# Performance work log

Hardware: AMD Instinct MI355X
Metric: run time of the kernel (lower is better)

Reference implementation:

```python
import jax, jax.numpy as jnp
import numpy as np
from jax import lax

D_MODEL = 768
D_STATE = 16
D_CONV = 4
EXPAND = 2
D_INNER = EXPAND * D_MODEL  # 1536
DT_RANK = (D_MODEL + 15) // 16  # 48
BATCH = 4
SEQ_LEN = 2048


def setup_inputs() -> dict:
    key = jax.random.key(0)
    ks = jax.random.split(key, 8)
    x = jax.random.normal(ks[0], (BATCH, SEQ_LEN, D_MODEL), dtype=jnp.float32)
    W_in = jax.random.normal(ks[1], (D_INNER * 2, D_MODEL), dtype=jnp.float32) * 0.02
    conv_w = jax.random.normal(ks[2], (D_INNER, 1, D_CONV), dtype=jnp.float32) * 0.1
    conv_b = jnp.zeros((D_INNER,), dtype=jnp.float32)
    W_x = jax.random.normal(ks[3], (DT_RANK + 2 * D_STATE, D_INNER), dtype=jnp.float32) * 0.02
    dt_std = DT_RANK ** -0.5
    W_dt = jax.random.uniform(ks[4], (D_INNER, DT_RANK), minval=-dt_std, maxval=dt_std, dtype=jnp.float32)
    b_dt = jnp.zeros((D_INNER,), dtype=jnp.float32)
    A_log = jnp.log(jnp.tile(jnp.arange(1, D_STATE + 1, dtype=jnp.float32), (D_INNER, 1)))
    D_param = jnp.ones((D_INNER,), dtype=jnp.float32)
    W_out = jax.random.normal(ks[5], (D_MODEL, D_INNER), dtype=jnp.float32) * 0.02
    return {"x": x, "W_in": W_in, "conv_w": conv_w, "conv_b": conv_b,
            "W_x": W_x, "W_dt": W_dt, "b_dt": b_dt, "A_log": A_log,
            "D_param": D_param, "W_out": W_out}


def _silu(v):
    return v * jax.nn.sigmoid(v)


def reference(x, W_in, conv_w, conv_b, W_x, W_dt, b_dt, A_log, D_param, W_out):
    B, L, _ = x.shape
    # in_proj and split into x-branch / gate z
    xz = jnp.einsum('bld,ed->ble', x, W_in)            # (B, L, 2*d_inner)
    xb, z = jnp.split(xz, 2, axis=-1)
    # depthwise causal conv1d (torch pads both sides then truncates to L)
    xc = jnp.transpose(xb, (0, 2, 1))                   # (B, d_inner, L)
    xc = lax.conv_general_dilated(xc, conv_w, window_strides=(1,),
                                  padding=[(D_CONV - 1, 0)],
                                  feature_group_count=D_INNER,
                                  dimension_numbers=('NCH', 'OIH', 'NCH'))
    xc = xc + conv_b[None, :, None]
    xc = jnp.transpose(xc, (0, 2, 1))                   # (B, L, d_inner)
    xc = _silu(xc)
    # ssm input-dependent params
    x_dbl = jnp.einsum('bld,ed->ble', xc, W_x)          # (B, L, dt_rank+2*d_state)
    dt_r = x_dbl[..., :DT_RANK]
    Bm = x_dbl[..., DT_RANK:DT_RANK + D_STATE]          # (B, L, d_state)
    Cm = x_dbl[..., DT_RANK + D_STATE:]
    dt = jax.nn.softplus(jnp.einsum('blr,dr->bld', dt_r, W_dt) + b_dt)
    A = -jnp.exp(A_log)                                 # (d_inner, d_state)
    # selective scan over time
    def step(h, inp):
        x_t, dt_t, B_t, C_t = inp                       # (B,d_inner),(B,d_inner),(B,d_state),(B,d_state)
        dA = jnp.exp(dt_t[..., None] * A)               # (B, d_inner, d_state)
        h = dA * h + (dt_t * x_t)[..., None] * B_t[:, None, :]
        y_t = jnp.einsum('bdn,bn->bd', h, C_t) + D_param * x_t
        return h, y_t
    h0 = jnp.zeros((B, D_INNER, D_STATE), dtype=x.dtype)
    xs = (jnp.transpose(xc, (1, 0, 2)), jnp.transpose(dt, (1, 0, 2)),
          jnp.transpose(Bm, (1, 0, 2)), jnp.transpose(Cm, (1, 0, 2)))
    _, ys = lax.scan(step, h0, xs)                      # (L, B, d_inner)
    y = jnp.transpose(ys, (1, 0, 2))
    y = y * _silu(z)
    return jnp.einsum('bld,od->blo', y, W_out)
```

## Files before the change

### kernel.cpp

```cpp
#include <hip/hip_runtime.h>
#include <hip/hip_bf16.h>
#include <math.h>

#define D_MODEL   768
#define D_STATE   16
#define D_CONV    4
#define D_INNER   1536
#define DT_RANK   48
#define BATCH     4
#define SEQ_LEN   2048
#define BL        (BATCH * SEQ_LEN)
#define NCHUNK    32
#define CHUNK     (SEQ_LEN / NCHUNK)

typedef __bf16 bf16x8 __attribute__((ext_vector_type(8)));
typedef float  f32x4  __attribute__((ext_vector_type(4)));

__device__ __forceinline__ void async_copy16(const void* g, void* l) {
    __builtin_amdgcn_global_load_lds(
        (const __attribute__((address_space(1))) void*)g,
        (__attribute__((address_space(3))) void*)l,
        16, 0, 0);
}


#define SYNC_V6 do { asm volatile("s_waitcnt vmcnt(6)" ::: "memory"); \
    __builtin_amdgcn_s_barrier(); __builtin_amdgcn_sched_barrier(0); } while (0)
#define SYNC_V4 do { asm volatile("s_waitcnt vmcnt(4)" ::: "memory"); \
    __builtin_amdgcn_s_barrier(); __builtin_amdgcn_sched_barrier(0); } while (0)
#define SYNC_V2 do { asm volatile("s_waitcnt vmcnt(2)" ::: "memory"); \
    __builtin_amdgcn_s_barrier(); __builtin_amdgcn_sched_barrier(0); } while (0)
#define SYNC_V0 do { asm volatile("s_waitcnt vmcnt(0)" ::: "memory"); \
    __builtin_amdgcn_s_barrier(); __builtin_amdgcn_sched_barrier(0); } while (0)
#define SYNC_B  do { \
    __builtin_amdgcn_s_barrier(); __builtin_amdgcn_sched_barrier(0); } while (0)

template<int IH, int JH>
__device__ __forceinline__ void quad24(f32x4 (&acc)[2][4][2][2],
                                       const bf16x8 (&aH)[4], const bf16x8 (&aL)[4],
                                       const bf16x8 (&bH)[2], const bf16x8 (&bL)[2])
{
    __builtin_amdgcn_s_setprio(1);
    #pragma unroll
    for (int i = 0; i < 4; ++i)
        #pragma unroll
        for (int j = 0; j < 2; ++j) {
            acc[IH][i][JH][j] = __builtin_amdgcn_mfma_f32_16x16x32_bf16(aH[i], bH[j], acc[IH][i][JH][j], 0, 0, 0);
            acc[IH][i][JH][j] = __builtin_amdgcn_mfma_f32_16x16x32_bf16(aH[i], bL[j], acc[IH][i][JH][j], 0, 0, 0);
            acc[IH][i][JH][j] = __builtin_amdgcn_mfma_f32_16x16x32_bf16(aL[i], bH[j], acc[IH][i][JH][j], 0, 0, 0);
        }
    __builtin_amdgcn_s_setprio(0);
}

__global__ __launch_bounds__(512, 2)
void gemm256(const __bf16* __restrict__ A, const __bf16* __restrict__ B,
             float* __restrict__ C, int K, int ldc)
{
    __shared__ __bf16 Asl0[256 * 64];
    __shared__ __bf16 Bsl0[256 * 64];
    __shared__ __bf16 Asl1[256 * 64];
    __shared__ __bf16 Bsl1[256 * 64];

    const int tid  = threadIdx.x;
    const int lane = tid & 63;
    const int w    = tid >> 6;
    const int aw   = (w >> 2) * 64;
    const int bw   = (w & 3) * 32;

    const int bm = blockIdx.y * 256;
    const int bn = blockIdx.x * 256;

    const long lda = 2L * K;
    const long ldb = 2L * K;

    f32x4 acc[2][4][2][2];
    #pragma unroll
    for (int a = 0; a < 2; ++a)
        #pragma unroll
        for (int i = 0; i < 4; ++i)
            #pragma unroll
            for (int b = 0; b < 2; ++b)
                #pragma unroll
                for (int j = 0; j < 2; ++j)
                    acc[a][i][b][j] = (f32x4){0.f, 0.f, 0.f, 0.f};

    const int srow = w * 8 + (lane >> 3);
    const int q    = (lane & 7) ^ ((lane >> 3) & 7);
    const int qoff = (q < 4) ? q * 8 : K + (q - 4) * 8;
    const __bf16* Ab = A + (long)(bm + srow) * lda + qoff;
    const __bf16* Bb = B + (long)(bn + srow) * ldb + qoff;
    const long lda64 = 64 * lda, ldb64 = 64 * ldb;
    const int wo = w * 1024;

    const int fr = lane & 15;
    const int g4 = lane >> 4;

    const int nt = K >> 5;

    __bf16 *Ac = Asl0, *Bc = Bsl0, *An = Asl1, *Bn = Bsl1;

    auto stA = [&](int kk, __bf16* dst, int half) {
        char* d = (char*)dst + half * 16384 + wo;
        const __bf16* s = Ab + kk + (long)(2 * half) * lda64;
        async_copy16(s, d);
        async_copy16(s + lda64, d + 8192);
    };
    auto stB = [&](int kk, __bf16* dst, int half) {
        char* d = (char*)dst + half * 16384 + wo;
        const __bf16* s = Bb + kk + (long)(2 * half) * ldb64;
        async_copy16(s, d);
        async_copy16(s + ldb64, d + 8192);
    };
    auto rdA = [&](const __bf16* As, int ih, bf16x8 (&aH)[4], bf16x8 (&aL)[4]) {
        #pragma unroll
        for (int t = 0; t < 4; ++t) {
            const int ra = aw + ih * 128 + t * 16 + fr;
            aH[t] = *(const bf16x8*)&As[ra * 64 + ((g4       ^ (ra & 7)) * 8)];
            aL[t] = *(const bf16x8*)&As[ra * 64 + (((4 + g4) ^ (ra & 7)) * 8)];
        }
    };
    auto rdB = [&](const __bf16* Bs, int jh, bf16x8 (&bH)[2], bf16x8 (&bL)[2]) {
        #pragma unroll
        for (int t = 0; t < 2; ++t) {
            const int rb = bw + jh * 128 + t * 16 + fr;
            bH[t] = *(const bf16x8*)&Bs[rb * 64 + ((g4       ^ (rb & 7)) * 8)];
            bL[t] = *(const bf16x8*)&Bs[rb * 64 + (((4 + g4) ^ (rb & 7)) * 8)];
        }
    };

    stA(0, Ac, 0);
    stB(0, Bc, 0);
    stB(0, Bc, 1);
    stA(0, Ac, 1);
    SYNC_V4;

    for (int t = 0; t < nt - 1; ++t) {
        const int kk1 = (t + 1) * 32;
        bf16x8 aH[4], aL[4], bH[2], bL[2];
        rdA(Ac, 0, aH, aL);
        rdB(Bc, 0, bH, bL);
        stA(kk1, An, 0);
        SYNC_V6;
        quad24<0, 0>(acc, aH, aL, bH, bL);
        rdB(Bc, 1, bH, bL);
        stB(kk1, Bn, 0);
        SYNC_V6;
        quad24<0, 1>(acc, aH, aL, bH, bL);
        rdA(Ac, 1, aH, aL);
        stB(kk1, Bn, 1);
        SYNC_V6;
        quad24<1, 1>(acc, aH, aL, bH, bL);
        rdB(Bc, 0, bH, bL);
        stA(kk1, An, 1);
        SYNC_B;
        quad24<1, 0>(acc, aH, aL, bH, bL);
        __bf16* tp;
        tp = Ac; Ac = An; An = tp;
        tp = Bc; Bc = Bn; Bn = tp;
    }

    {
        bf16x8 aH[4], aL[4], bH[2], bL[2];
        rdA(Ac, 0, aH, aL);
        rdB(Bc, 0, bH, bL);
        SYNC_V4;
        quad24<0, 0>(acc, aH, aL, bH, bL);
        rdB(Bc, 1, bH, bL);
        SYNC_V2;
        quad24<0, 1>(acc, aH, aL, bH, bL);
        rdA(Ac, 1, aH, aL);
        SYNC_V0;
        quad24<1, 1>(acc, aH, aL, bH, bL);
        rdB(Bc, 0, bH, bL);
        quad24<1, 0>(acc, aH, aL, bH, bL);
    }

    const int cn  = lane & 15;
    const int cr4 = (lane >> 4) * 4;
    #pragma unroll
    for (int ih = 0; ih < 2; ++ih)
        #pragma unroll
        for (int i = 0; i < 4; ++i)
            #pragma unroll
            for (int jh = 0; jh < 2; ++jh)
                #pragma unroll
                for (int j = 0; j < 2; ++j)
                    #pragma unroll
                    for (int r = 0; r < 4; ++r) {
                        const int row = bm + aw + ih * 128 + i * 16 + cr4 + r;
                        const int col = bn + bw + jh * 128 + j * 16 + cn;
                        C[(long)row * ldc + col] = acc[ih][i][jh][j][r];
                    }
}

template <int EPI>
__global__ __launch_bounds__(256)
void gemm_f(const __bf16* __restrict__ A, const __bf16* __restrict__ B,
            float* __restrict__ C, const float* __restrict__ bias,
            int M, int N, int K, int ldc)
{
    __shared__ __bf16 Asl[128 * 64];
    __shared__ __bf16 Bsl[128 * 64];

    const int tid  = threadIdx.x;
    const int lane = tid & 63;
    const int w    = tid >> 6;
    const int wm   = (w >> 1) * 64;
    const int wn   = (w & 1) * 64;

    const int bm = blockIdx.y * 128;
    const int bn = blockIdx.x * 128;

    const long lda = 2L * K;
    const long ldb = 2L * K;

    f32x4 acc[4][4];
    #pragma unroll
    for (int i = 0; i < 4; ++i)
        #pragma unroll
        for (int j = 0; j < 4; ++j)
            acc[i][j] = (f32x4){0.f, 0.f, 0.f, 0.f};

    const int srow = w * 32 + (lane >> 3);
    const int q    = (lane & 7) ^ ((lane >> 3) & 7);
    const int qoff = (q < 4) ? q * 8 : K + (q - 4) * 8;
    const __bf16* Abase = A + (long)(bm + srow) * lda + qoff;
    const __bf16* Bbase = B + (long)(bn + srow) * ldb + qoff;
    char* AslW = (char*)Asl + (w * 32) * 128;
    char* BslW = (char*)Bsl + (w * 32) * 128;

    const int fr = lane & 15;
    const int g4 = lane >> 4;
    const long lda8 = 8 * lda, ldb8 = 8 * ldb;

    for (int kk = 0; kk < K; kk += 32) {
        __syncthreads();
        #pragma unroll
        for (int j = 0; j < 4; ++j) {
            async_copy16(Abase + j * lda8 + kk, AslW + j * 1024);
            async_copy16(Bbase + j * ldb8 + kk, BslW + j * 1024);
        }
        __syncthreads();

        bf16x8 ah[4], al[4], bh[4], bl[4];
        #pragma unroll
        for (int t = 0; t < 4; ++t) {
            const int ra = wm + t * 16 + fr;
            const int rb = wn + t * 16 + fr;
            ah[t] = *(const bf16x8*)&Asl[ra * 64 + ((g4       ^ (ra & 7)) * 8)];
            al[t] = *(const bf16x8*)&Asl[ra * 64 + (((4 + g4) ^ (ra & 7)) * 8)];
            bh[t] = *(const bf16x8*)&Bsl[rb * 64 + ((g4       ^ (rb & 7)) * 8)];
            bl[t] = *(const bf16x8*)&Bsl[rb * 64 + (((4 + g4) ^ (rb & 7)) * 8)];
        }
        #pragma unroll
        for (int i = 0; i < 4; ++i)
            #pragma unroll
            for (int j = 0; j < 4; ++j) {
                acc[i][j] = __builtin_amdgcn_mfma_f32_16x16x32_bf16(ah[i], bh[j], acc[i][j], 0, 0, 0);
                acc[i][j] = __builtin_amdgcn_mfma_f32_16x16x32_bf16(ah[i], bl[j], acc[i][j], 0, 0, 0);
                acc[i][j] = __builtin_amdgcn_mfma_f32_16x16x32_bf16(al[i], bh[j], acc[i][j], 0, 0, 0);
            }
    }

    const int cn  = lane & 15;
    const int cr4 = (lane >> 4) * 4;
    #pragma unroll
    for (int i = 0; i < 4; ++i)
        #pragma unroll
        for (int j = 0; j < 4; ++j)
            #pragma unroll
            for (int r = 0; r < 4; ++r) {
                const int row = bm + wm + i * 16 + cr4 + r;
                const int col = bn + wn + j * 16 + cn;
                float v = acc[i][j][r];
                if (EPI == 1) {
                    v += bias[col];
                    v = fmaxf(v, 0.f) + log1pf(__expf(-fabsf(v)));
                }
                C[(long)row * ldc + col] = v;
            }
}

__global__ __launch_bounds__(256)
void gemm_xdbl(const __bf16* __restrict__ A, const __bf16* __restrict__ B,
               float* __restrict__ xdtP, float* __restrict__ xbc)
{
    __shared__ __bf16 Asl[128 * 64];
    __shared__ __bf16 Bsl[128 * 64];

    const int tid  = threadIdx.x;
    const int lane = tid & 63;
    const int w    = tid >> 6;
    const int wm   = (w >> 1) * 64;
    const int wn   = (w & 1) * 64;

    const int s  = blockIdx.x;
    const int bm = blockIdx.y * 128;
    const int K  = 1536;
    const long lda = 3072, ldb = 3072;

    f32x4 acc[4][4];
    #pragma unroll
    for (int i = 0; i < 4; ++i)
        #pragma unroll
        for (int j = 0; j < 4; ++j)
            acc[i][j] = (f32x4){0.f, 0.f, 0.f, 0.f};

    const int srow = w * 32 + (lane >> 3);
    const int q    = (lane & 7) ^ ((lane >> 3) & 7);
    const int qoff = (q < 4) ? q * 8 : K + (q - 4) * 8;
    const __bf16* Abase = A + (long)(bm + srow) * lda + qoff;
    const __bf16* Bbase = B + (long)srow * ldb + qoff;
    char* AslW = (char*)Asl + (w * 32) * 128;
    char* BslW = (char*)Bsl + (w * 32) * 128;

    const int fr = lane & 15;
    const int g4 = lane >> 4;
    const long lda8 = 8 * lda, ldb8 = 8 * ldb;

    for (int kt = s * 12; kt < (s + 1) * 12; ++kt) {
        const int kk = kt * 32;
        __syncthreads();
        #pragma unroll
        for (int j = 0; j < 4; ++j) {
            async_copy16(Abase + j * lda8 + kk, AslW + j * 1024);
            async_copy16(Bbase + j * ldb8 + kk, BslW + j * 1024);
        }
        __syncthreads();

        bf16x8 ah[4], al[4], bh[4], bl[4];
        #pragma unroll
        for (int t = 0; t < 4; ++t) {
            const int ra = wm + t * 16 + fr;
            const int rb = wn + t * 16 + fr;
            ah[t] = *(const bf16x8*)&Asl[ra * 64 + ((g4       ^ (ra & 7)) * 8)];
            al[t] = *(const bf16x8*)&Asl[ra * 64 + (((4 + g4) ^ (ra & 7)) * 8)];
            bh[t] = *(const bf16x8*)&Bsl[rb * 64 + ((g4       ^ (rb & 7)) * 8)];
            bl[t] = *(const bf16x8*)&Bsl[rb * 64 + (((4 + g4) ^ (rb & 7)) * 8)];
        }
        #pragma unroll
        for (int i = 0; i < 4; ++i)
            #pragma unroll
            for (int j = 0; j < 4; ++j) {
                acc[i][j] = __builtin_amdgcn_mfma_f32_16x16x32_bf16(ah[i], bh[j], acc[i][j], 0, 0, 0);
                acc[i][j] = __builtin_amdgcn_mfma_f32_16x16x32_bf16(ah[i], bl[j], acc[i][j], 0, 0, 0);
                acc[i][j] = __builtin_amdgcn_mfma_f32_16x16x32_bf16(al[i], bh[j], acc[i][j], 0, 0, 0);
            }
    }

    const int cn  = lane & 15;
    const int cr4 = (lane >> 4) * 4;
    #pragma unroll
    for (int i = 0; i < 4; ++i)
        #pragma unroll
        for (int j = 0; j < 4; ++j) {
            const int col = wn + j * 16 + cn;
            if (col >= 80) continue;
            #pragma unroll
            for (int r = 0; r < 4; ++r) {
                const int row = bm + wm + i * 16 + cr4 + r;
                const float v = acc[i][j][r];
                if (col < 48) atomicAdd(&xdtP[(long)row * 48 + col], v);
                else          atomicAdd(&xbc [(long)row * 32 + (col - 48)], v);
            }
        }
}

__global__ __launch_bounds__(256)
void zero_xp(float* __restrict__ xbc, float* __restrict__ xdtP)
{
    const long i = (long)blockIdx.x * 256 + threadIdx.x;
    if (i < 8192L * 32) xbc[i]  = 0.f;
    if (i < 8192L * 48) xdtP[i] = 0.f;
}

__global__ __launch_bounds__(256)
void xdt_split(const float* __restrict__ xdtP, __bf16* __restrict__ xdtS)
{
    const long i = (long)blockIdx.x * 256 + threadIdx.x;
    if (i >= 8192L * 128) return;
    const long r = i >> 7;
    const int  c = (int)(i & 127);
    const int  k = c & 63;
    const float u = (k < 48) ? xdtP[r * 48 + k] : 0.f;
    const __bf16 hi = (__bf16)u;
    xdtS[i] = (c < 64) ? hi : (__bf16)(u - (float)hi);
}

#define NW0 ((long)BL * 768)
#define NW1 (3072L * 768)
#define NW2 (768L * 1536)
#define NW3 (80L * 1536)
#define NW4 (1536L * 128)
__global__ __launch_bounds__(256)
void split_all(const float* __restrict__ x,
               const float* __restrict__ W_in, const float* __restrict__ W_out,
               const float* __restrict__ W_x, const float* __restrict__ W_dt,
               __bf16* __restrict__ xS,
               __bf16* __restrict__ wInS, __bf16* __restrict__ wOutS,
               __bf16* __restrict__ wXS, __bf16* __restrict__ wDtS)
{
    long i = (long)blockIdx.x * 256 + threadIdx.x;
    if (i < NW0) {
        const long row = i / 768; const int col = (int)(i - row * 768);
        const float a = x[i];
        const __bf16 h = (__bf16)a;
        __bf16* d = xS + row * 1536 + col;
        d[0] = h; d[768] = (__bf16)(a - (float)h);
        return;
    }
    i -= NW0;
    if (i < NW1) {
        const long row = i / 768; const int col = (int)(i - row * 768);
        const float a = W_in[i];
        const __bf16 h = (__bf16)a;
        __bf16* d = wInS + row * 1536 + col;
        d[0] = h; d[768] = (__bf16)(a - (float)h);
        return;
    }
    i -= NW1;
    if (i < NW2) {
        const long row = i / 1536; const int col = (int)(i - row * 1536);
        const float a = W_out[i];
        const __bf16 h = (__bf16)a;
        __bf16* d = wOutS + row * 3072 + col;
        d[0] = h; d[1536] = (__bf16)(a - (float)h);
        return;
    }
    i -= NW2;
    if (i < NW3) {
        const long row = i / 1536; const int col = (int)(i - row * 1536);
        const float a = W_x[i];
        const __bf16 h = (__bf16)a;
        __bf16* d = wXS + row * 3072 + col;
        d[0] = h; d[1536] = (__bf16)(a - (float)h);
        return;
    }
    i -= NW3;
    if (i < NW4) {
        const long row = i >> 7; const int c = (int)(i & 127);
        const int k = c & 63;
        const float a = (k < 48) ? W_dt[row * 48 + k] : 0.f;
        const __bf16 h = (__bf16)a;
        wDtS[row * 128 + c] = (c < 64) ? h : (__bf16)(a - (float)h);
    }
}

typedef __bf16 bf16x4 __attribute__((ext_vector_type(4)));

__global__ __launch_bounds__(256)
void conv_silu_kernel(const float* __restrict__ xz,
                      const float* __restrict__ conv_w,
                      const float* __restrict__ conv_b,
                      __bf16* __restrict__ xcS)
{
    const long idx = (long)blockIdx.x * 256 + threadIdx.x;
    const int d4 = (int)(idx % (D_INNER / 4)) * 4;
    const long bl = idx / (D_INNER / 4);
    const int l  = (int)(bl % SEQ_LEN);

    const f32x4 w0 = *(const f32x4*)&conv_w[(d4 + 0) * 4];
    const f32x4 w1 = *(const f32x4*)&conv_w[(d4 + 1) * 4];
    const f32x4 w2 = *(const f32x4*)&conv_w[(d4 + 2) * 4];
    const f32x4 w3 = *(const f32x4*)&conv_w[(d4 + 3) * 4];
    const f32x4 bb = *(const f32x4*)&conv_b[d4];

    const float* base = xz + bl * 3072 + d4;
    f32x4 t0 = {0.f,0.f,0.f,0.f}, t1 = t0, t2 = t0, t3;
    if (l >= 3) t0 = *(const f32x4*)(base - 3 * 3072);
    if (l >= 2) t1 = *(const f32x4*)(base - 2 * 3072);
    if (l >= 1) t2 = *(const f32x4*)(base - 1 * 3072);
    t3 = *(const f32x4*)base;

    bf16x4 hi4, lo4;
    #pragma unroll
    for (int e = 0; e < 4; ++e) {
        const f32x4 we = (e == 0) ? w0 : (e == 1) ? w1 : (e == 2) ? w2 : w3;
        float s = bb[e];
        s = fmaf(t0[e], we[0], s);
        s = fmaf(t1[e], we[1], s);
        s = fmaf(t2[e], we[2], s);
        s = fmaf(t3[e], we[3], s);
        const float sig = 1.f / (1.f + __expf(-s));
        const float v = s * sig;
        const __bf16 h = (__bf16)v;
        hi4[e] = h;
        lo4[e] = (__bf16)(v - (float)h);
    }
    *(bf16x4*)&xcS[bl * 3072 + d4]        = hi4;
    *(bf16x4*)&xcS[bl * 3072 + 1536 + d4] = lo4;
}

__global__ __launch_bounds__(256)
void scan_phaseA(const __bf16* __restrict__ xcS, const float* __restrict__ xz,
                 const float* __restrict__ xbc, const float* __restrict__ A_log,
                 float* __restrict__ P, float* __restrict__ S)
{
    const int d = blockIdx.x * 256 + threadIdx.x;
    const int c = blockIdx.y;
    const int b = blockIdx.z;

    float An[16], Pr[16], Sr[16];
    #pragma unroll
    for (int n = 0; n < 16; ++n) {
        An[n] = -__expf(A_log[d * 16 + n]);
        Pr[n] = 1.f;
        Sr[n] = 0.f;
    }

    const long bl0 = (long)b * SEQ_LEN + (long)c * CHUNK;
    #pragma unroll 4
    for (int l = 0; l < CHUNK; ++l) {
        const long bl = bl0 + l;
        const float dt  = xz[bl * 3072 + d];
        const float x   = (float)xcS[bl * 3072 + d] + (float)xcS[bl * 3072 + 1536 + d];
        const float dtx = dt * x;
        float bcr[16];
        #pragma unroll
        for (int v = 0; v < 4; ++v)
            *(f32x4*)&bcr[v * 4] = *(const f32x4*)&xbc[bl * 32 + v * 4];
        #pragma unroll
        for (int n = 0; n < 16; ++n) {
            const float a = __expf(dt * An[n]);
            Pr[n] *= a;
            Sr[n] = fmaf(a, Sr[n], dtx * bcr[n]);
        }
    }

    const long base = ((long)(b * NCHUNK + c) * 16) * D_INNER + d;
    #pragma unroll
    for (int n = 0; n < 16; ++n) {
        P[base + (long)n * D_INNER] = Pr[n];
        S[base + (long)n * D_INNER] = Sr[n];
    }
}

__global__ __launch_bounds__(256)
void scan_phaseB(const float* __restrict__ P, const float* __restrict__ S,
                 float* __restrict__ H)
{
    const int t = blockIdx.x * 256 + threadIdx.x;
    const int d = t % D_INNER;
    const int r = t / D_INNER;
    const int n = r & 15;
    const int b = r >> 4;

    float h = 0.f;
    for (int c = 0; c < NCHUNK; ++c) {
        const long i = ((long)(b * NCHUNK + c) * 16 + n) * D_INNER + d;
        H[i] = h;
        h = fmaf(P[i], h, S[i]);
    }
}

__global__ __launch_bounds__(256)
void scan_phaseC(__bf16* xcS_yS, const float* __restrict__ xz,
                 const float* __restrict__ xbc, const float* __restrict__ A_log,
                 const float* __restrict__ Dp, const float* __restrict__ H)
{
    const int d = blockIdx.x * 256 + threadIdx.x;
    const int c = blockIdx.y;
    const int b = blockIdx.z;

    float An[16], h[16];
    const long hbase = ((long)(b * NCHUNK + c) * 16) * D_INNER + d;
    #pragma unroll
    for (int n = 0; n < 16; ++n) {
        An[n] = -__expf(A_log[d * 16 + n]);
        h[n]  = H[hbase + (long)n * D_INNER];
    }
    const float Dd = Dp[d];

    const long bl0 = (long)b * SEQ_LEN + (long)c * CHUNK;
    #pragma unroll 2
    for (int l = 0; l < CHUNK; ++l) {
        const long bl = bl0 + l;
        const float dt  = xz[bl * 3072 + d];
        const float x   = (float)xcS_yS[bl * 3072 + d] + (float)xcS_yS[bl * 3072 + 1536 + d];
        const float dtx = dt * x;
        float bcr[32];
        #pragma unroll
        for (int v = 0; v < 8; ++v)
            *(f32x4*)&bcr[v * 4] = *(const f32x4*)&xbc[bl * 32 + v * 4];
        float y = Dd * x;
        #pragma unroll
        for (int n = 0; n < 16; ++n) {
            const float a = __expf(dt * An[n]);
            h[n] = fmaf(a, h[n], dtx * bcr[n]);
            y = fmaf(h[n], bcr[16 + n], y);
        }
        const float z  = xz[bl * 3072 + D_INNER + d];
        const float sz = z / (1.f + __expf(-z));
        const float v  = y * sz;
        const __bf16 hi = (__bf16)v;
        const __bf16 lo = (__bf16)(v - (float)hi);
        xcS_yS[bl * 3072 + d]        = hi;
        xcS_yS[bl * 3072 + 1536 + d] = lo;
    }
}

extern "C" void kernel_launch(void* const* d_in, const int* in_sizes, int n_in,
                              void* d_out, int out_size, void* d_ws, size_t ws_size,
                              hipStream_t stream)
{
    const float* x      = (const float*)d_in[0];
    const float* W_in   = (const float*)d_in[1];
    const float* conv_w = (const float*)d_in[2];
    const float* conv_b = (const float*)d_in[3];
    const float* W_x    = (const float*)d_in[4];
    const float* W_dt   = (const float*)d_in[5];
    const float* b_dt   = (const float*)d_in[6];
    const float* A_log  = (const float*)d_in[7];
    const float* D_p    = (const float*)d_in[8];
    const float* W_out  = (const float*)d_in[9];
    float* out = (float*)d_out;

    char* p = (char*)d_ws;
    auto take = [&](size_t bytes) { char* r = p; p += (bytes + 255) & ~(size_t)255; return r; };

    float*  xz    = (float*)take((size_t)BL * 3072 * 4);
    float*  H     = (float*)take((size_t)BATCH * NCHUNK * 16 * D_INNER * 4);
    __bf16* wOutS = (__bf16*)take(768L * 3072 * 2);
    __bf16* wXS   = (__bf16*)take(128L * 3072 * 2);
    __bf16* wDtS  = (__bf16*)take(1536L * 128 * 2);
    __bf16* xdtS  = (__bf16*)take(8192L * 128 * 2);
    float*  xdtP  = (float*)take(8192L * 48 * 4);
    float*  xbc   = (float*)take(8192L * 32 * 4);
    float*  Pout  = (float*)take(4L * 8192 * 128 * 4);
    float*  S     = (float*)take((size_t)BATCH * NCHUNK * 16 * D_INNER * 4);
    float*  P     = Pout;

    char* region = take(50331648);
    __bf16* xS   = (__bf16*)region;
    __bf16* wInS = (__bf16*)(region + 25165824);
    __bf16* xcS  = (__bf16*)region;
    __bf16* yS   = (__bf16*)region;

    {
        const long n = NW0 + NW1 + NW2 + NW3 + NW4;
        split_all<<<(int)((n + 255) / 256), 256, 0, stream>>>(
            x, W_in, W_out, W_x, W_dt, xS, wInS, wOutS, wXS, wDtS);
    }
    {
        dim3 grid(3072 / 256, BL / 256);
        gemm256<<<grid, 512, 0, stream>>>(xS, wInS, xz, 768, 3072);
    }
    {
        const long total = (long)BL * (D_INNER / 4);
        conv_silu_kernel<<<(int)(total / 256), 256, 0, stream>>>(xz, conv_w, conv_b, xcS);
    }
    zero_xp<<<(int)((8192L * 48 + 255) / 256), 256, 0, stream>>>(xbc, xdtP);
    {
        dim3 grid(4, BL / 128);
        gemm_xdbl<<<grid, 256, 0, stream>>>(xcS, wXS, xdtP, xbc);
    }
    {
        const long n = 8192L * 128;
        xdt_split<<<(int)((n + 255) / 256), 256, 0, stream>>>(xdtP, xdtS);
    }
    {
        dim3 grid(1536 / 128, BL / 128);
        gemm_f<1><<<grid, 256, 0, stream>>>(xdtS, wDtS, xz, b_dt,
                                            BL, 1536, 64, 3072);
    }
    {
        dim3 grid(D_INNER / 256, NCHUNK, BATCH);
        scan_phaseA<<<grid, 256, 0, stream>>>(xcS, xz, xbc, A_log, P, S);
    }
    scan_phaseB<<<(BATCH * 16 * D_INNER) / 256, 256, 0, stream>>>(P, S, H);
    {
        dim3 grid(D_INNER / 256, NCHUNK, BATCH);
        scan_phaseC<<<grid, 256, 0, stream>>>(xcS, xz, xbc, A_log, D_p, H);
    }
    {
        dim3 grid(768 / 128, BL / 128);
        gemm_f<0><<<grid, 256, 0, stream>>>(yS, wOutS, out, nullptr,
                                            BL, 768, 1536, 768);
    }
}
```

Measured before the change: 513.8 us.

## Fuse dt projection and softplus into scan phases, drop dt GEMM

The separate dt GEMM (split-bf16 MFMA) and its input split kernel are removed. Each scan thread now holds its 48-wide W_dt row in registers and computes dt = softplus(xdtP·W_dt + b_dt) per timestep inside both phase A and phase C. This avoids writing and re-reading the 8192x1536 dt tensor and drops two launches. In exchange it recomputes the projection twice with scalar FMAs, adds 48 registers per thread, and reads B/C values directly from global memory without vector loads.

```diff
diff --git a/kernel.cpp b/kernel.cpp
--- a/kernel.cpp
+++ b/kernel.cpp
@@ -193,11 +193,9 @@
                     }
 }
 
-template <int EPI>
 __global__ __launch_bounds__(256)
 void gemm_f(const __bf16* __restrict__ A, const __bf16* __restrict__ B,
-            float* __restrict__ C, const float* __restrict__ bias,
-            int M, int N, int K, int ldc)
+            float* __restrict__ C, int M, int N, int K, int ldc)
 {
     __shared__ __bf16 Asl[128 * 64];
     __shared__ __bf16 Bsl[128 * 64];
@@ -272,12 +270,7 @@
             for (int r = 0; r < 4; ++r) {
                 const int row = bm + wm + i * 16 + cr4 + r;
                 const int col = bn + wn + j * 16 + cn;
-                float v = acc[i][j][r];
-                if (EPI == 1) {
-                    v += bias[col];
-                    v = fmaxf(v, 0.f) + log1pf(__expf(-fabsf(v)));
-                }
-                C[(long)row * ldc + col] = v;
+                C[(long)row * ldc + col] = acc[i][j][r];
             }
 }
 
@@ -374,31 +367,17 @@
     if (i < 8192L * 48) xdtP[i] = 0.f;
 }
 
-__global__ __launch_bounds__(256)
-void xdt_split(const float* __restrict__ xdtP, __bf16* __restrict__ xdtS)
-{
-    const long i = (long)blockIdx.x * 256 + threadIdx.x;
-    if (i >= 8192L * 128) return;
-    const long r = i >> 7;
-    const int  c = (int)(i & 127);
-    const int  k = c & 63;
-    const float u = (k < 48) ? xdtP[r * 48 + k] : 0.f;
-    const __bf16 hi = (__bf16)u;
-    xdtS[i] = (c < 64) ? hi : (__bf16)(u - (float)hi);
-}
-
 #define NW0 ((long)BL * 768)
 #define NW1 (3072L * 768)
 #define NW2 (768L * 1536)
 #define NW3 (80L * 1536)
-#define NW4 (1536L * 128)
 __global__ __launch_bounds__(256)
 void split_all(const float* __restrict__ x,
                const float* __restrict__ W_in, const float* __restrict__ W_out,
-               const float* __restrict__ W_x, const float* __restrict__ W_dt,
+               const float* __restrict__ W_x,
                __bf16* __restrict__ xS,
                __bf16* __restrict__ wInS, __bf16* __restrict__ wOutS,
-               __bf16* __restrict__ wXS, __bf16* __restrict__ wDtS)
+               __bf16* __restrict__ wXS)
 {
     long i = (long)blockIdx.x * 256 + threadIdx.x;
     if (i < NW0) {
@@ -434,15 +413,6 @@
         const __bf16 h = (__bf16)a;
         __bf16* d = wXS + row * 3072 + col;
         d[0] = h; d[1536] = (__bf16)(a - (float)h);
-        return;
-    }
-    i -= NW3;
-    if (i < NW4) {
-        const long row = i >> 7; const int c = (int)(i & 127);
-        const int k = c & 63;
-        const float a = (k < 48) ? W_dt[row * 48 + k] : 0.f;
-        const __bf16 h = (__bf16)a;
-        wDtS[row * 128 + c] = (c < 64) ? h : (__bf16)(a - (float)h);
     }
 }
 
@@ -491,14 +461,30 @@
     *(bf16x4*)&xcS[bl * 3072 + 1536 + d4] = lo4;
 }
 
-__global__ __launch_bounds__(256)
-void scan_phaseA(const __bf16* __restrict__ xcS, const float* __restrict__ xz,
+__device__ __forceinline__ float fused_dt(const float* __restrict__ xr,
+                                          const float (&wdt)[48], float bdt)
+{
+    float s = bdt;
+    #pragma unroll
+    for (int k = 0; k < 48; ++k) s = fmaf(xr[k], wdt[k], s);
+    return fmaxf(s, 0.f) + log1pf(__expf(-fabsf(s)));
+}
+
+__global__ __launch_bounds__(256)
+void scan_phaseA(const __bf16* __restrict__ xcS, const float* __restrict__ xdtP,
+                 const float* __restrict__ W_dt, const float* __restrict__ b_dt,
                  const float* __restrict__ xbc, const float* __restrict__ A_log,
                  float* __restrict__ P, float* __restrict__ S)
 {
     const int d = blockIdx.x * 256 + threadIdx.x;
     const int c = blockIdx.y;
     const int b = blockIdx.z;
+
+    float wdt[48];
+    #pragma unroll
+    for (int k = 0; k < 48; k += 4)
+        *(f32x4*)&wdt[k] = *(const f32x4*)&W_dt[(long)d * 48 + k];
+    const float bdt = b_dt[d];
 
     float An[16], Pr[16], Sr[16];
     #pragma unroll
@@ -509,21 +495,17 @@
     }
 
     const long bl0 = (long)b * SEQ_LEN + (long)c * CHUNK;
-    #pragma unroll 4
     for (int l = 0; l < CHUNK; ++l) {
         const long bl = bl0 + l;
-        const float dt  = xz[bl * 3072 + d];
-        const float x   = (float)xcS[bl * 3072 + d] + (float)xcS[bl * 3072 + 1536 + d];
+        const float dt = fused_dt(xdtP + bl * 48, wdt, bdt);
+        const float x  = (float)xcS[bl * 3072 + d] + (float)xcS[bl * 3072 + 1536 + d];
         const float dtx = dt * x;
-        float bcr[16];
-        #pragma unroll
-        for (int v = 0; v < 4; ++v)
-            *(f32x4*)&bcr[v * 4] = *(const f32x4*)&xbc[bl * 32 + v * 4];
+        const float* bc = xbc + bl * 32;
         #pragma unroll
         for (int n = 0; n < 16; ++n) {
             const float a = __expf(dt * An[n]);
             Pr[n] *= a;
-            Sr[n] = fmaf(a, Sr[n], dtx * bcr[n]);
+            Sr[n] = fmaf(a, Sr[n], dtx * bc[n]);
         }
     }
 
@@ -555,6 +537,8 @@
 
 __global__ __launch_bounds__(256)
 void scan_phaseC(__bf16* xcS_yS, const float* __restrict__ xz,
+                 const float* __restrict__ xdtP,
+                 const float* __restrict__ W_dt, const float* __restrict__ b_dt,
                  const float* __restrict__ xbc, const float* __restrict__ A_log,
                  const float* __restrict__ Dp, const float* __restrict__ H)
 {
@@ -562,6 +546,12 @@
     const int c = blockIdx.y;
     const int b = blockIdx.z;
 
+    float wdt[48];
+    #pragma unroll
+    for (int k = 0; k < 48; k += 4)
+        *(f32x4*)&wdt[k] = *(const f32x4*)&W_dt[(long)d * 48 + k];
+    const float bdt = b_dt[d];
+
     float An[16], h[16];
     const long hbase = ((long)(b * NCHUNK + c) * 16) * D_INNER + d;
     #pragma unroll
@@ -572,22 +562,18 @@
     const float Dd = Dp[d];
 
     const long bl0 = (long)b * SEQ_LEN + (long)c * CHUNK;
-    #pragma unroll 2
     for (int l = 0; l < CHUNK; ++l) {
         const long bl = bl0 + l;
-        const float dt  = xz[bl * 3072 + d];
-        const float x   = (float)xcS_yS[bl * 3072 + d] + (float)xcS_yS[bl * 3072 + 1536 + d];
+        const float dt = fused_dt(xdtP + bl * 48, wdt, bdt);
+        const float x  = (float)xcS_yS[bl * 3072 + d] + (float)xcS_yS[bl * 3072 + 1536 + d];
         const float dtx = dt * x;
-        float bcr[32];
-        #pragma unroll
-        for (int v = 0; v < 8; ++v)
-            *(f32x4*)&bcr[v * 4] = *(const f32x4*)&xbc[bl * 32 + v * 4];
+        const float* bc = xbc + bl * 32;
         float y = Dd * x;
         #pragma unroll
         for (int n = 0; n < 16; ++n) {
             const float a = __expf(dt * An[n]);
-            h[n] = fmaf(a, h[n], dtx * bcr[n]);
-            y = fmaf(h[n], bcr[16 + n], y);
+            h[n] = fmaf(a, h[n], dtx * bc[n]);
+            y = fmaf(h[n], bc[16 + n], y);
         }
         const float z  = xz[bl * 3072 + D_INNER + d];
         const float sz = z / (1.f + __expf(-z));
@@ -622,8 +608,6 @@
     float*  H     = (float*)take((size_t)BATCH * NCHUNK * 16 * D_INNER * 4);
     __bf16* wOutS = (__bf16*)take(768L * 3072 * 2);
     __bf16* wXS   = (__bf16*)take(128L * 3072 * 2);
-    __bf16* wDtS  = (__bf16*)take(1536L * 128 * 2);
-    __bf16* xdtS  = (__bf16*)take(8192L * 128 * 2);
     float*  xdtP  = (float*)take(8192L * 48 * 4);
     float*  xbc   = (float*)take(8192L * 32 * 4);
     float*  Pout  = (float*)take(4L * 8192 * 128 * 4);
@@ -637,9 +621,9 @@
     __bf16* yS   = (__bf16*)region;
 
     {
-        const long n = NW0 + NW1 + NW2 + NW3 + NW4;
+        const long n = NW0 + NW1 + NW2 + NW3;
         split_all<<<(int)((n + 255) / 256), 256, 0, stream>>>(
-            x, W_in, W_out, W_x, W_dt, xS, wInS, wOutS, wXS, wDtS);
+            x, W_in, W_out, W_x, xS, wInS, wOutS, wXS);
     }
     {
         dim3 grid(3072 / 256, BL / 256);
@@ -655,26 +639,18 @@
         gemm_xdbl<<<grid, 256, 0, stream>>>(xcS, wXS, xdtP, xbc);
     }
     {
-        const long n = 8192L * 128;
-        xdt_split<<<(int)((n + 255) / 256), 256, 0, stream>>>(xdtP, xdtS);
-    }
-    {
-        dim3 grid(1536 / 128, BL / 128);
-        gemm_f<1><<<grid, 256, 0, stream>>>(xdtS, wDtS, xz, b_dt,
-                                            BL, 1536, 64, 3072);
-    }
-    {
         dim3 grid(D_INNER / 256, NCHUNK, BATCH);
-        scan_phaseA<<<grid, 256, 0, stream>>>(xcS, xz, xbc, A_log, P, S);
+        scan_phaseA<<<grid, 256, 0, stream>>>(xcS, xdtP, W_dt, b_dt,
+                                              xbc, A_log, P, S);
     }
     scan_phaseB<<<(BATCH * 16 * D_INNER) / 256, 256, 0, stream>>>(P, S, H);
     {
         dim3 grid(D_INNER / 256, NCHUNK, BATCH);
-        scan_phaseC<<<grid, 256, 0, stream>>>(xcS, xz, xbc, A_log, D_p, H);
+        scan_phaseC<<<grid, 256, 0, stream>>>(xcS, xz, xdtP, W_dt, b_dt,
+                                              xbc, A_log, D_p, H);
     }
     {
         dim3 grid(768 / 128, BL / 128);
-        gemm_f<0><<<grid, 256, 0, stream>>>(yS, wOutS, out, nullptr,
-                                            BL, 768, 1536, 768);
-    }
-}
+        gemm_f<<<grid, 256, 0, stream>>>(yS, wOutS, out, BL, 768, 1536, 768);
+    }
+}
```

After: 583.7 us. +13.6%, slower.
